# Kernel optimization log

Hardware: AMD Instinct MI355X
Metric: run time of the kernel (lower is better)

## Reference

```python
import jax, jax.numpy as jnp
import numpy as np

EPS = 1e-05

def exp_map_at_origin(v, c):
    sqrt_c = jnp.sqrt(c)
    v_norm = jnp.maximum(jnp.linalg.norm(v, axis=-1, keepdims=True), EPS)
    return (1.0 / sqrt_c) * jnp.tanh(sqrt_c * v_norm) * (v / v_norm)

def log_map_at_origin(y, c):
    sqrt_c = jnp.sqrt(c)
    y_norm = jnp.maximum(jnp.linalg.norm(y, axis=-1, keepdims=True), EPS)
    y_norm_clamped = jnp.minimum(y_norm, 1.0 / sqrt_c - EPS)
    return (1.0 / sqrt_c) * jnp.arctanh(sqrt_c * y_norm_clamped) * (y / y_norm)

def poincare_distance(x, y, c):
    # x, y: [B, H, S, d]; returns [B, H, S, S]
    sqrt_c = jnp.sqrt(c)
    xns = jnp.sum(x * x, axis=-1, keepdims=True)          # [B,H,S,1]
    yns = jnp.sum(y * y, axis=-1, keepdims=True)          # [B,H,S,1]
    xy = jnp.einsum('bhsd,bhtd->bhst', x, y)
    xnsb = xns                                            # broadcast over t
    ynsb = jnp.swapaxes(yns, -2, -1)                      # [B,H,1,S]
    diff_norm_sq = xnsb - 2.0 * xy + ynsb
    denom = jnp.maximum((1.0 - c * xnsb) * (1.0 - c * ynsb), EPS)
    arg = jnp.maximum(1.0 + 2.0 * c * diff_norm_sq / denom, 1.0 + EPS)
    return (1.0 / sqrt_c) * jnp.arccosh(arg)

def setup_inputs() -> dict:
    key = jax.random.key(0)
    ks = jax.random.split(key, 5)
    B, S, D = 2, 1024, 1024
    x = jax.random.normal(ks[0], (B, S, D), dtype=jnp.float32)
    scale = 0.02
    W_q = scale * jax.random.normal(ks[1], (D, D), dtype=jnp.float32)
    W_k = scale * jax.random.normal(ks[2], (D, D), dtype=jnp.float32)
    W_v = scale * jax.random.normal(ks[3], (D, D), dtype=jnp.float32)
    W_o = scale * jax.random.normal(ks[4], (D, D), dtype=jnp.float32)
    return {
        'x': x, 'W_q': W_q, 'W_k': W_k, 'W_v': W_v, 'W_o': W_o,
        'log_c': jnp.zeros((), jnp.float32),
        'beta': jnp.zeros((), jnp.float32),
        'attention_bias': jnp.zeros((), jnp.float32),
    }

def reference(x, W_q, W_k, W_v, W_o, log_c, beta, attention_bias):
    B, S, D = x.shape
    H = 16
    dh = D // H
    c = jax.nn.softplus(log_c)
    beta_pos = jax.nn.softplus(beta)

    def split_heads(t):  # [B,S,D] -> [B,H,S,dh]
        return jnp.transpose(t.reshape(B, S, H, dh), (0, 2, 1, 3))

    q_t = split_heads(x @ W_q.T)
    k_t = split_heads(x @ W_k.T)
    v_t = split_heads(x @ W_v.T)

    q_h = exp_map_at_origin(q_t, c)
    k_h = exp_map_at_origin(k_t, c)
    v_h = exp_map_at_origin(v_t, c)

    dist = poincare_distance(q_h, k_h, c)                 # [B,H,S,S]
    scores = -beta_pos * dist - attention_bias
    weights = jax.nn.softmax(scores, axis=-1)

    v_tan = log_map_at_origin(v_h, c)
    out_tan = jnp.einsum('bhst,bhtd->bhsd', weights, v_tan)
    out_hyp = exp_map_at_origin(out_tan, c)
    out_heads_tan = log_map_at_origin(out_hyp, c)

    concat = jnp.transpose(out_heads_tan, (0, 2, 1, 3)).reshape(B, S, D)
    return concat @ W_o.T
```

## Files before the change

### kernel.cpp

```cpp
#include <hip/hip_runtime.h>
#include <math.h>


#define EPS_ 1e-5f

constexpr int Ss = 1024, Dd = 1024, Hh = 16, DHh = 64;

typedef __attribute__((ext_vector_type(8))) short bf16x8;
typedef __attribute__((ext_vector_type(4))) short s16x4;
typedef __attribute__((ext_vector_type(4))) float f32x4;

__device__ __forceinline__ float softplusf_(float x) {
    return (x > 20.f) ? x : log1pf(expf(x));
}
__device__ __forceinline__ float waveSum64(float v) {
#pragma unroll
    for (int m = 32; m >= 1; m >>= 1) v += __shfl_xor(v, m, 64);
    return v;
}
__device__ __forceinline__ short f2bf(float f) {
    union { float f; unsigned u; } v; v.f = f;
    unsigned r = v.u + 0x7FFFu + ((v.u >> 16) & 1u);
    return (short)(r >> 16);
}
__device__ __forceinline__ float bf2f(unsigned short h) {
    union { unsigned u; float f; } v; v.u = ((unsigned)h) << 16;
    return v.f;
}
__device__ __forceinline__ unsigned pks(short a, short b) {
    return (unsigned)(unsigned short)a | ((unsigned)(unsigned short)b << 16);
}

#if __has_builtin(__builtin_amdgcn_cvt_pk_bf16_f32)
typedef __attribute__((ext_vector_type(2))) __bf16 bfp2;
__device__ __forceinline__ unsigned cvtpk(float a, float b) {
    union { bfp2 v; unsigned u; } x;
    x.v = __builtin_amdgcn_cvt_pk_bf16_f32(a, b);
    return x.u;
}
#else
__device__ __forceinline__ unsigned cvtpk(float a, float b) { return pks(f2bf(a), f2bf(b)); }
#endif

#if __has_builtin(__builtin_amdgcn_sqrtf)
#define FSQRT __builtin_amdgcn_sqrtf
#else
#define FSQRT sqrtf
#endif
#if __has_builtin(__builtin_amdgcn_logf)
#define FLOG2 __builtin_amdgcn_logf
#else
#define FLOG2 __log2f
#endif
#if __has_builtin(__builtin_amdgcn_exp2f)
#define FEXP2 __builtin_amdgcn_exp2f
#else
#define FEXP2 exp2f
#endif

__device__ __forceinline__ void gload_lds16(const short* gp, short* lp) {
    __builtin_amdgcn_global_load_lds(
        (__attribute__((address_space(1))) void*)(void*)(const_cast<short*>(gp)),
        (__attribute__((address_space(3))) void*)(void*)(lp), 16, 0, 0);
}

__global__ __launch_bounds__(256) void split_all(
    const float* __restrict__ x,  const float* __restrict__ Wq,
    const float* __restrict__ Wk, const float* __restrict__ Wv,
    const float* __restrict__ Wo,
    short* __restrict__ xh,  short* __restrict__ wqh,
    short* __restrict__ wkh, short* __restrict__ wvh, short* __restrict__ woh)
{
    int g = blockIdx.x * 256 + threadIdx.x;
    const float* src; short* dst; int base;
    if (g < 524288)       { src = x;  dst = xh;  base = g; }
    else if (g < 786432)  { src = Wq; dst = wqh; base = g - 524288; }
    else if (g < 1048576) { src = Wk; dst = wkh; base = g - 786432; }
    else if (g < 1310720) { src = Wv; dst = wvh; base = g - 1048576; }
    else                  { src = Wo; dst = woh; base = g - 1310720; }
    float4 v = *(const float4*)(src + (size_t)base * 4);
    uint2 hp; hp.x = cvtpk(v.x, v.y); hp.y = cvtpk(v.z, v.w);
    *(uint2*)(dst + (size_t)base * 4) = hp;
}

__global__ __launch_bounds__(256, 3) void gemm_qkv(
    const short* __restrict__ Ap,
    const short* __restrict__ Wq, const short* __restrict__ Wk, const short* __restrict__ Wv,
    short* __restrict__ qh, short* __restrict__ kh, short* __restrict__ vtT,
    float* __restrict__ qnsT, float2* __restrict__ knpk,
    const float* __restrict__ p_logc)
{
    const int z = blockIdx.z;
    const short* Bp = (z == 0) ? Wq : (z == 1 ? Wk : Wv);
    const int K = 1024;

    __shared__ short As[128 * 64];
    __shared__ short Bs[64 * 64];

    const int tid = threadIdx.x;
    const int wv = tid >> 6, lane = tid & 63, quad = lane >> 4, l15 = lane & 15;
    const int bm = blockIdx.y * 128, bn = blockIdx.x * 64;

    const int lr8 = lane >> 3, lc8 = lane & 7;
    const int swz8 = (lc8 ^ lr8) * 8;

    const short* gAl = Ap + (size_t)(bm + lr8) * K + swz8;
    const short* gBl = Bp + (size_t)(bn + lr8) * K + swz8;

    f32x4 acc[2][4];
#pragma unroll
    for (int mt = 0; mt < 2; mt++)
#pragma unroll
        for (int j = 0; j < 4; j++) acc[mt][j] = (f32x4){0.f, 0.f, 0.f, 0.f};

    for (int k0 = 0; k0 < K; k0 += 64) {
        __syncthreads();
#pragma unroll
        for (int i = 0; i < 4; i++)
            gload_lds16(gAl + (size_t)((wv * 4 + i) * 8) * K + k0, &As[(wv * 4 + i) * 512]);
#pragma unroll
        for (int j = 0; j < 2; j++)
            gload_lds16(gBl + (size_t)((wv * 2 + j) * 8) * K + k0, &Bs[(wv * 2 + j) * 512]);
        __syncthreads();
#pragma unroll
        for (int w = 0; w < 2; w++) {
            const int xs = ((w * 4 + quad) ^ (l15 & 7)) * 8;
            bf16x8 fa0 = *(const bf16x8*)&As[(wv * 32 + l15) * 64 + xs];
            bf16x8 fa1 = *(const bf16x8*)&As[(wv * 32 + 16 + l15) * 64 + xs];
#pragma unroll
            for (int nt = 0; nt < 4; nt++) {
                bf16x8 fb = *(const bf16x8*)&Bs[(nt * 16 + l15) * 64 + xs];
                acc[0][nt] = __builtin_amdgcn_mfma_f32_16x16x32_bf16(fa0, fb, acc[0][nt], 0, 0, 0);
                acc[1][nt] = __builtin_amdgcn_mfma_f32_16x16x32_bf16(fa1, fb, acc[1][nt], 0, 0, 0);
            }
        }
    }

    const float c = softplusf_(p_logc[0]);
    const float sc = sqrtf(c);
    const float twoC = 2.f * c;
    const int h0 = blockIdx.x;

    if (z < 2) {
        short* yout = (z == 0) ? qh : kh;
#pragma unroll
        for (int mt = 0; mt < 2; mt++) {
            const int mbase = bm + wv * 32 + mt * 16;
            float fr[4];
#pragma unroll
            for (int r = 0; r < 4; r++) {
                float s2 = 0.f;
#pragma unroll
                for (int nt = 0; nt < 4; nt++) s2 += acc[mt][nt][r] * acc[mt][nt][r];
#pragma unroll
                for (int mk = 1; mk < 16; mk <<= 1) s2 += __shfl_xor(s2, mk, 64);
                float n = fmaxf(sqrtf(s2), EPS_);
                float fac = tanhf(sc * n) / (sc * n);
                fr[r] = fac;
                if (l15 == 0) {
                    int m = mbase + quad * 4 + r;
                    int bI = m >> 10, s = m & 1023;
                    float yns = s2 * fac * fac;
                    if (z == 0) {
                        qnsT[(size_t)(bI * Hh + h0) * Ss + s] = yns;
                    } else {
                        knpk[(size_t)(bI * Hh + h0) * Ss + s]
                            = make_float2(yns, twoC / (1.f - c * yns));
                    }
                }
            }
#pragma unroll
            for (int nt = 0; nt < 4; nt++)
#pragma unroll
                for (int r = 0; r < 4; r++) {
                    int m = mbase + quad * 4 + r;
                    yout[(size_t)m * Dd + bn + nt * 16 + l15] = f2bf(acc[mt][nt][r] * fr[r]);
                }
        }
    } else {
#pragma unroll
        for (int mt = 0; mt < 2; mt++) {
            const int mbase = bm + wv * 32 + mt * 16;
            float tr[4];
#pragma unroll
            for (int r = 0; r < 4; r++) {
                float s2 = 0.f;
#pragma unroll
                for (int nt = 0; nt < 4; nt++) s2 += acc[mt][nt][r] * acc[mt][nt][r];
#pragma unroll
                for (int mk = 1; mk < 16; mk <<= 1) s2 += __shfl_xor(s2, mk, 64);
                float n = fmaxf(sqrtf(s2), EPS_);
                float fac = tanhf(sc * n) / (sc * n);
                float yn = n * fac;
                float ycl = fminf(yn, 1.f / sc - EPS_);
                float f2 = atanhf(sc * ycl) / (sc * fmaxf(yn, EPS_));
                tr[r] = fac * f2;
            }
            const int m0 = mbase + quad * 4;
            const int bI = m0 >> 10, s0 = m0 & 1023;
            const int w6 = s0 & 63;
            const int s0p = (s0 & ~63)
                          | ((w6 >> 5) * 32 + ((w6 & 15) >> 2) * 8 + ((w6 >> 4) & 1) * 4);
#pragma unroll
            for (int nt = 0; nt < 4; nt++) {
                int d = nt * 16 + l15;
                uint2 pk;
                pk.x = cvtpk(acc[mt][nt][0] * tr[0], acc[mt][nt][1] * tr[1]);
                pk.y = cvtpk(acc[mt][nt][2] * tr[2], acc[mt][nt][3] * tr[3]);
                *(uint2*)&vtT[((size_t)(bI * Hh + h0) * DHh + d) * Ss + s0p] = pk;
            }
        }
    }
}

__global__ __launch_bounds__(256) void attn_mfma(
    const short* __restrict__ qh, const short* __restrict__ kh, const short* __restrict__ vtT,
    const float* __restrict__ qnsT, const float2* __restrict__ knpk,
    unsigned short* __restrict__ Opart, float* __restrict__ lpart,
    const float* __restrict__ p_logc, const float* __restrict__ p_beta)
{
    const float c = softplusf_(p_logc[0]);
    const float sc = sqrtf(c);
    const float bp = softplusf_(p_beta[0]);
    const float nkc = -bp / sc;
    const float cap = 2.f * c * 1e5f;
    const float onePlus = 1.f + EPS_;

    const int h = blockIdx.y, b = blockIdx.z;
    const int kr = blockIdx.x & 1, qt = blockIdx.x >> 1;
    const int tid = threadIdx.x;
    const int wv = tid >> 6, lane = tid & 63;
    const int quad = lane >> 4, l15 = lane & 15;
    const int bh = b * Hh + h;
    const int q = qt * 64 + wv * 16 + l15;

    __shared__ short Ks[2][64 * 64];
    __shared__ short Vt[2][64 * 64];

    const short* qb = qh + (size_t)(b * Ss + q) * Dd + h * DHh + quad * 8;
    bf16x8 qf0 = *(const bf16x8*)qb;
    bf16x8 qf1 = *(const bf16x8*)(qb + 32);

    const float qn = qnsT[(size_t)bh * Ss + q];
    const float irq = 1.f / (1.f - c * qn);

    f32x4 O4[4];
#pragma unroll
    for (int nt = 0; nt < 4; nt++) O4[nt] = (f32x4){0.f, 0.f, 0.f, 0.f};
    float lac = 0.f;

    const int tbase = kr * 512;
    const int lr8 = lane >> 3, lc8 = lane & 7;
    const float2* nb = knpk + (size_t)bh * Ss;
    const short* ksb = kh + (size_t)b * Ss * Dd + h * DHh + (lc8 ^ lr8) * 8;
    const short* vsb = vtT + (size_t)bh * DHh * Ss + tbase + (lc8 ^ lr8) * 8;

#pragma unroll
    for (int j = 0; j < 2; j++) {
        const int R = wv * 16 + j * 8;
        gload_lds16(ksb + (size_t)(tbase + R + lr8) * Dd, &Ks[0][R * 64]);
        gload_lds16(vsb + (size_t)(R + lr8) * Ss, &Vt[0][R * 64]);
    }
    __syncthreads();

    const int xsl = (quad ^ (l15 & 7)) * 8;

    for (int ch = 0; ch < 8; ch++) {
        const int cur = ch & 1, nxt = cur ^ 1;
        const int t0 = tbase + ch * 64;

        if (ch < 7) {
#pragma unroll
            for (int j = 0; j < 2; j++) {
                const int R = wv * 16 + j * 8;
                gload_lds16(ksb + (size_t)(tbase + (ch + 1) * 64 + R + lr8) * Dd,
                            &Ks[nxt][R * 64]);
                gload_lds16(vsb + (size_t)(R + lr8) * Ss + (ch + 1) * 64,
                            &Vt[nxt][R * 64]);
            }
        }

        f32x4 n0[4], n1[4];
#pragma unroll
        for (int nt = 0; nt < 4; nt++) {
            const float2* np = nb + t0 + nt * 16 + quad * 4;
            n0[nt] = *(const f32x4*)np;
            n1[nt] = *(const f32x4*)(np + 2);
        }

        f32x4 acc[4];
#pragma unroll
        for (int nt = 0; nt < 4; nt++) {
            bf16x8 k0 = *(const bf16x8*)&Ks[cur][(nt * 16 + l15) * 64 + xsl];
            bf16x8 k1 = *(const bf16x8*)&Ks[cur][(nt * 16 + l15) * 64 + (xsl ^ 32)];
            f32x4 a = (f32x4){0.f, 0.f, 0.f, 0.f};
            a = __builtin_amdgcn_mfma_f32_16x16x32_bf16(k0, qf0, a, 0, 0, 0);
            a = __builtin_amdgcn_mfma_f32_16x16x32_bf16(k1, qf1, a, 0, 0, 0);
            acc[nt] = a;
        }

        bf16x8 v0[4], v1[4];
#pragma unroll
        for (int nt = 0; nt < 4; nt++) {
            v0[nt] = *(const bf16x8*)&Vt[cur][(nt * 16 + l15) * 64 + xsl];
            v1[nt] = *(const bf16x8*)&Vt[cur][(nt * 16 + l15) * 64 + (xsl ^ 32)];
        }

        float sv[4][4];
#pragma unroll
        for (int nt = 0; nt < 4; nt++) {
#pragma unroll
            for (int r = 0; r < 4; r++) {
                float kn   = (r < 2) ? n0[nt][(r & 1) * 2]     : n1[nt][(r & 1) * 2];
                float ik2c = (r < 2) ? n0[nt][(r & 1) * 2 + 1] : n1[nt][(r & 1) * 2 + 1];
                float dns = (qn + kn) - 2.f * acc[nt][r];
                float co  = fminf(irq * ik2c, cap);
                float arg = fmaxf(fmaf(co, dns, 1.f), onePlus);
                float u   = arg + FSQRT(fmaf(arg, arg, -1.f));
                float p   = FEXP2(nkc * FLOG2(u));
                sv[nt][r] = p;
                lac += p;
            }
        }

        union { unsigned u[4]; bf16x8 v; } p0, p1;
        p0.u[0] = cvtpk(sv[0][0], sv[0][1]); p0.u[1] = cvtpk(sv[0][2], sv[0][3]);
        p0.u[2] = cvtpk(sv[1][0], sv[1][1]); p0.u[3] = cvtpk(sv[1][2], sv[1][3]);
        p1.u[0] = cvtpk(sv[2][0], sv[2][1]); p1.u[1] = cvtpk(sv[2][2], sv[2][3]);
        p1.u[2] = cvtpk(sv[3][0], sv[3][1]); p1.u[3] = cvtpk(sv[3][2], sv[3][3]);

#pragma unroll
        for (int nt = 0; nt < 4; nt++) {
            O4[nt] = __builtin_amdgcn_mfma_f32_16x16x32_bf16(v0[nt], p0.v, O4[nt], 0, 0, 0);
            O4[nt] = __builtin_amdgcn_mfma_f32_16x16x32_bf16(v1[nt], p1.v, O4[nt], 0, 0, 0);
        }

        if (ch < 7) __syncthreads();
    }

    lac += __shfl_xor(lac, 16, 64);
    lac += __shfl_xor(lac, 32, 64);
    unsigned short* ob = Opart + (((size_t)bh * 2 + kr) * Ss + q) * DHh;
#pragma unroll
    for (int nt = 0; nt < 4; nt++) {
        uint2 pk;
        pk.x = cvtpk(O4[nt][0], O4[nt][1]);
        pk.y = cvtpk(O4[nt][2], O4[nt][3]);
        *(uint2*)(ob + nt * 16 + quad * 4) = pk;
    }
    if (lane < 16)
        lpart[((size_t)bh * 2 + kr) * Ss + qt * 64 + wv * 16 + lane] = lac;
}

__global__ __launch_bounds__(256) void attn_combine(
    const unsigned short* __restrict__ Opart, const float* __restrict__ lpart,
    short* __restrict__ ccb, const float* __restrict__ p_logc)
{
    const float c = softplusf_(p_logc[0]);
    const float sc = sqrtf(c);
    const int wv = threadIdx.x >> 6, d = threadIdx.x & 63;
    const int task = blockIdx.x * 4 + wv;
    const int bh = task >> 10, s = task & 1023;

    float O = 0.f, l = 0.f;
#pragma unroll
    for (int k = 0; k < 2; k++) {
        O += bf2f(Opart[(((size_t)bh * 2 + k) * Ss + s) * DHh + d]);
        l += lpart[((size_t)bh * 2 + k) * Ss + s];
    }
    float ot = O / l;

    float t2 = waveSum64(ot * ot);
    float n = fmaxf(sqrtf(t2), EPS_);
    float fac = tanhf(sc * n) / (sc * n);
    float y2 = t2 * fac * fac;
    float yn = fmaxf(sqrtf(y2), EPS_);
    float ycl = fminf(yn, 1.f / sc - EPS_);
    float fac2 = atanhf(sc * ycl) / (sc * yn);
    float tot = fac * fac2;

    int b = bh >> 4, hh = bh & 15;
    ccb[(size_t)(b * Ss + s) * Dd + hh * DHh + d] = f2bf(ot * tot);
}

__global__ __launch_bounds__(256, 6) void gemm_out(
    const short* __restrict__ Ap, const short* __restrict__ Bp,
    float* __restrict__ Cp)
{
    const int K = 1024, N = 1024;
    __shared__ short As[64 * 64];
    __shared__ short Bs[64 * 64];
    const int tid = threadIdx.x;
    const int wv = tid >> 6, lane = tid & 63, quad = lane >> 4, l15 = lane & 15;
    const int bm = blockIdx.y * 64, bn = blockIdx.x * 64;

    const int lr8 = lane >> 3, lc8 = lane & 7;
    const int swz8 = (lc8 ^ lr8) * 8;

    const short* gAl = Ap + (size_t)(bm + lr8) * K + swz8;
    const short* gBl = Bp + (size_t)(bn + lr8) * K + swz8;

    f32x4 acc[4];
#pragma unroll
    for (int j = 0; j < 4; j++) acc[j] = (f32x4){0.f, 0.f, 0.f, 0.f};

    for (int k0 = 0; k0 < K; k0 += 64) {
        __syncthreads();
#pragma unroll
        for (int j = 0; j < 2; j++) {
            gload_lds16(gAl + (size_t)((wv * 2 + j) * 8) * K + k0, &As[(wv * 2 + j) * 512]);
            gload_lds16(gBl + (size_t)((wv * 2 + j) * 8) * K + k0, &Bs[(wv * 2 + j) * 512]);
        }
        __syncthreads();
#pragma unroll
        for (int w = 0; w < 2; w++) {
            const int xs = ((w * 4 + quad) ^ (l15 & 7)) * 8;
            bf16x8 fa = *(const bf16x8*)&As[(wv * 16 + l15) * 64 + xs];
#pragma unroll
            for (int nt = 0; nt < 4; nt++) {
                bf16x8 fb = *(const bf16x8*)&Bs[(nt * 16 + l15) * 64 + xs];
                acc[nt] = __builtin_amdgcn_mfma_f32_16x16x32_bf16(fa, fb, acc[nt], 0, 0, 0);
            }
        }
    }
#pragma unroll
    for (int nt = 0; nt < 4; nt++)
#pragma unroll
        for (int r = 0; r < 4; r++)
            Cp[(size_t)(bm + wv * 16 + quad * 4 + r) * N + bn + nt * 16 + l15] = acc[nt][r];
}

extern "C" void kernel_launch(void* const* d_in, const int* in_sizes, int n_in,
                              void* d_out, int out_size, void* d_ws, size_t ws_size,
                              hipStream_t stream)
{
    const float* x    = (const float*)d_in[0];
    const float* Wq   = (const float*)d_in[1];
    const float* Wk   = (const float*)d_in[2];
    const float* Wv   = (const float*)d_in[3];
    const float* Wo   = (const float*)d_in[4];
    const float* logc = (const float*)d_in[5];
    const float* beta = (const float*)d_in[6];
    float* out = (float*)d_out;

    const size_t M2 = 2097152, M1 = 1048576;
    short* ws    = (short*)d_ws;
    short* xh    = ws;
    short* wqh   = xh + M2;
    short* wkh   = wqh + M1;
    short* wvh   = wkh + M1;
    short* woh   = wvh + M1;
    short* qh    = woh + M1;
    short* kh    = qh + M2;
    short* vtT   = kh + M2;
    float* qnsT  = (float*)(vtT + M2);
    float2* knpk = (float2*)(qnsT + 32768);
    float* lpart = (float*)(knpk + 32768);
    unsigned short* Opart = (unsigned short*)(lpart + 65536);
    short* ccb   = xh;

    split_all<<<dim3(6144), 256, 0, stream>>>(x, Wq, Wk, Wv, Wo, xh, wqh, wkh, wvh, woh);
    gemm_qkv<<<dim3(16, 16, 3), 256, 0, stream>>>(xh, wqh, wkh, wvh,
        qh, kh, vtT, qnsT, knpk, logc);
    attn_mfma<<<dim3(32, 16, 2), 256, 0, stream>>>(qh, kh, vtT, qnsT, knpk,
        Opart, lpart, logc, beta);
    attn_combine<<<dim3(8192), 256, 0, stream>>>(Opart, lpart, ccb, logc);
    gemm_out<<<dim3(16, 32), 256, 0, stream>>>(ccb, woh, out);
}
```

Before: 174.1 us.

## Fuse split-K attention combine into attention kernel via intra-block LDS reduction

The two key-range halves that were separate blocks now run as two wave groups inside one 512-thread block. The partial outputs and row sums are reduced through shared memory, and the exp/log map epilogue is applied in-kernel, so the attn_combine launch and the Opart/lpart global round trip go away. s_setprio is also raised around the MFMA sections to favor matrix issue. The cost is a larger block with twice the LDS, half the number of blocks, and an extra shared-memory reduction step at the end.

```diff
diff --git a/kernel.cpp b/kernel.cpp
--- a/kernel.cpp
+++ b/kernel.cpp
@@ -12,20 +12,11 @@
 
 __device__ __forceinline__ float softplusf_(float x) {
     return (x > 20.f) ? x : log1pf(expf(x));
-}
-__device__ __forceinline__ float waveSum64(float v) {
-#pragma unroll
-    for (int m = 32; m >= 1; m >>= 1) v += __shfl_xor(v, m, 64);
-    return v;
 }
 __device__ __forceinline__ short f2bf(float f) {
     union { float f; unsigned u; } v; v.f = f;
     unsigned r = v.u + 0x7FFFu + ((v.u >> 16) & 1u);
     return (short)(r >> 16);
-}
-__device__ __forceinline__ float bf2f(unsigned short h) {
-    union { unsigned u; float f; } v; v.u = ((unsigned)h) << 16;
-    return v.f;
 }
 __device__ __forceinline__ unsigned pks(short a, short b) {
     return (unsigned)(unsigned short)a | ((unsigned)(unsigned short)b << 16);
@@ -213,10 +204,10 @@
     }
 }
 
-__global__ __launch_bounds__(256) void attn_mfma(
+__global__ __launch_bounds__(512) void attn_mfma(
     const short* __restrict__ qh, const short* __restrict__ kh, const short* __restrict__ vtT,
     const float* __restrict__ qnsT, const float2* __restrict__ knpk,
-    unsigned short* __restrict__ Opart, float* __restrict__ lpart,
+    short* __restrict__ ccb,
     const float* __restrict__ p_logc, const float* __restrict__ p_beta)
 {
     const float c = softplusf_(p_logc[0]);
@@ -226,16 +217,16 @@
     const float cap = 2.f * c * 1e5f;
     const float onePlus = 1.f + EPS_;
 
-    const int h = blockIdx.y, b = blockIdx.z;
-    const int kr = blockIdx.x & 1, qt = blockIdx.x >> 1;
+    const int h = blockIdx.y, b = blockIdx.z, qt = blockIdx.x;
     const int tid = threadIdx.x;
     const int wv = tid >> 6, lane = tid & 63;
+    const int g = wv >> 2, w4 = wv & 3;
     const int quad = lane >> 4, l15 = lane & 15;
     const int bh = b * Hh + h;
-    const int q = qt * 64 + wv * 16 + l15;
-
-    __shared__ short Ks[2][64 * 64];
-    __shared__ short Vt[2][64 * 64];
+    const int q = qt * 64 + w4 * 16 + l15;
+
+    __shared__ short Ks[2][2][4096];
+    __shared__ short Vt[2][2][4096];
 
     const short* qb = qh + (size_t)(b * Ss + q) * Dd + h * DHh + quad * 8;
     bf16x8 qf0 = *(const bf16x8*)qb;
@@ -249,7 +240,7 @@
     for (int nt = 0; nt < 4; nt++) O4[nt] = (f32x4){0.f, 0.f, 0.f, 0.f};
     float lac = 0.f;
 
-    const int tbase = kr * 512;
+    const int tbase = g * 512;
     const int lr8 = lane >> 3, lc8 = lane & 7;
     const float2* nb = knpk + (size_t)bh * Ss;
     const short* ksb = kh + (size_t)b * Ss * Dd + h * DHh + (lc8 ^ lr8) * 8;
@@ -257,9 +248,9 @@
 
 #pragma unroll
     for (int j = 0; j < 2; j++) {
-        const int R = wv * 16 + j * 8;
-        gload_lds16(ksb + (size_t)(tbase + R + lr8) * Dd, &Ks[0][R * 64]);
-        gload_lds16(vsb + (size_t)(R + lr8) * Ss, &Vt[0][R * 64]);
+        const int R = w4 * 16 + j * 8;
+        gload_lds16(ksb + (size_t)(tbase + R + lr8) * Dd, &Ks[g][0][R * 64]);
+        gload_lds16(vsb + (size_t)(R + lr8) * Ss, &Vt[g][0][R * 64]);
     }
     __syncthreads();
 
@@ -272,11 +263,11 @@
         if (ch < 7) {
 #pragma unroll
             for (int j = 0; j < 2; j++) {
-                const int R = wv * 16 + j * 8;
+                const int R = w4 * 16 + j * 8;
                 gload_lds16(ksb + (size_t)(tbase + (ch + 1) * 64 + R + lr8) * Dd,
-                            &Ks[nxt][R * 64]);
+                            &Ks[g][nxt][R * 64]);
                 gload_lds16(vsb + (size_t)(R + lr8) * Ss + (ch + 1) * 64,
-                            &Vt[nxt][R * 64]);
+                            &Vt[g][nxt][R * 64]);
             }
         }
 
@@ -289,21 +280,23 @@
         }
 
         f32x4 acc[4];
-#pragma unroll
-        for (int nt = 0; nt < 4; nt++) {
-            bf16x8 k0 = *(const bf16x8*)&Ks[cur][(nt * 16 + l15) * 64 + xsl];
-            bf16x8 k1 = *(const bf16x8*)&Ks[cur][(nt * 16 + l15) * 64 + (xsl ^ 32)];
+        __builtin_amdgcn_s_setprio(1);
+#pragma unroll
+        for (int nt = 0; nt < 4; nt++) {
+            bf16x8 k0 = *(const bf16x8*)&Ks[g][cur][(nt * 16 + l15) * 64 + xsl];
+            bf16x8 k1 = *(const bf16x8*)&Ks[g][cur][(nt * 16 + l15) * 64 + (xsl ^ 32)];
             f32x4 a = (f32x4){0.f, 0.f, 0.f, 0.f};
             a = __builtin_amdgcn_mfma_f32_16x16x32_bf16(k0, qf0, a, 0, 0, 0);
             a = __builtin_amdgcn_mfma_f32_16x16x32_bf16(k1, qf1, a, 0, 0, 0);
             acc[nt] = a;
         }
+        __builtin_amdgcn_s_setprio(0);
 
         bf16x8 v0[4], v1[4];
 #pragma unroll
         for (int nt = 0; nt < 4; nt++) {
-            v0[nt] = *(const bf16x8*)&Vt[cur][(nt * 16 + l15) * 64 + xsl];
-            v1[nt] = *(const bf16x8*)&Vt[cur][(nt * 16 + l15) * 64 + (xsl ^ 32)];
+            v0[nt] = *(const bf16x8*)&Vt[g][cur][(nt * 16 + l15) * 64 + xsl];
+            v1[nt] = *(const bf16x8*)&Vt[g][cur][(nt * 16 + l15) * 64 + (xsl ^ 32)];
         }
 
         float sv[4][4];
@@ -329,58 +322,66 @@
         p1.u[0] = cvtpk(sv[2][0], sv[2][1]); p1.u[1] = cvtpk(sv[2][2], sv[2][3]);
         p1.u[2] = cvtpk(sv[3][0], sv[3][1]); p1.u[3] = cvtpk(sv[3][2], sv[3][3]);
 
+        __builtin_amdgcn_s_setprio(1);
 #pragma unroll
         for (int nt = 0; nt < 4; nt++) {
             O4[nt] = __builtin_amdgcn_mfma_f32_16x16x32_bf16(v0[nt], p0.v, O4[nt], 0, 0, 0);
             O4[nt] = __builtin_amdgcn_mfma_f32_16x16x32_bf16(v1[nt], p1.v, O4[nt], 0, 0, 0);
         }
+        __builtin_amdgcn_s_setprio(0);
 
         if (ch < 7) __syncthreads();
     }
 
     lac += __shfl_xor(lac, 16, 64);
     lac += __shfl_xor(lac, 32, 64);
-    unsigned short* ob = Opart + (((size_t)bh * 2 + kr) * Ss + q) * DHh;
-#pragma unroll
-    for (int nt = 0; nt < 4; nt++) {
-        uint2 pk;
-        pk.x = cvtpk(O4[nt][0], O4[nt][1]);
-        pk.y = cvtpk(O4[nt][2], O4[nt][3]);
-        *(uint2*)(ob + nt * 16 + quad * 4) = pk;
-    }
-    if (lane < 16)
-        lpart[((size_t)bh * 2 + kr) * Ss + qt * 64 + wv * 16 + lane] = lac;
-}
-
-__global__ __launch_bounds__(256) void attn_combine(
-    const unsigned short* __restrict__ Opart, const float* __restrict__ lpart,
-    short* __restrict__ ccb, const float* __restrict__ p_logc)
-{
-    const float c = softplusf_(p_logc[0]);
-    const float sc = sqrtf(c);
-    const int wv = threadIdx.x >> 6, d = threadIdx.x & 63;
-    const int task = blockIdx.x * 4 + wv;
-    const int bh = task >> 10, s = task & 1023;
-
-    float O = 0.f, l = 0.f;
-#pragma unroll
-    for (int k = 0; k < 2; k++) {
-        O += bf2f(Opart[(((size_t)bh * 2 + k) * Ss + s) * DHh + d]);
-        l += lpart[((size_t)bh * 2 + k) * Ss + s];
-    }
-    float ot = O / l;
-
-    float t2 = waveSum64(ot * ot);
-    float n = fmaxf(sqrtf(t2), EPS_);
-    float fac = tanhf(sc * n) / (sc * n);
-    float y2 = t2 * fac * fac;
-    float yn = fmaxf(sqrtf(y2), EPS_);
-    float ycl = fminf(yn, 1.f / sc - EPS_);
-    float fac2 = atanhf(sc * ycl) / (sc * yn);
-    float tot = fac * fac2;
-
-    int b = bh >> 4, hh = bh & 15;
-    ccb[(size_t)(b * Ss + s) * Dd + hh * DHh + d] = f2bf(ot * tot);
+
+    float* Ored = (float*)&Ks[0][0][0];
+    float* lred = (float*)&Vt[0][0][0];
+    __syncthreads();
+    if (g == 1) {
+#pragma unroll
+        for (int nt = 0; nt < 4; nt++)
+#pragma unroll
+            for (int r = 0; r < 4; r++)
+                Ored[((w4 * 4 + nt) * 16 + (quad * 4 + r)) * 16 + l15] = O4[nt][r];
+        if (lane < 16) lred[w4 * 16 + lane] = lac;
+    }
+    __syncthreads();
+
+    if (g == 0) {
+        const float lt = lac + lred[w4 * 16 + l15];
+        const float il = 1.f / lt;
+        float ot[4][4], t2 = 0.f;
+#pragma unroll
+        for (int nt = 0; nt < 4; nt++)
+#pragma unroll
+            for (int r = 0; r < 4; r++) {
+                float v = (O4[nt][r]
+                    + Ored[((w4 * 4 + nt) * 16 + (quad * 4 + r)) * 16 + l15]) * il;
+                ot[nt][r] = v;
+                t2 += v * v;
+            }
+        t2 += __shfl_xor(t2, 16, 64);
+        t2 += __shfl_xor(t2, 32, 64);
+
+        float n = fmaxf(sqrtf(t2), EPS_);
+        float fac = tanhf(sc * n) / (sc * n);
+        float y2 = t2 * fac * fac;
+        float yn = fmaxf(sqrtf(y2), EPS_);
+        float ycl = fminf(yn, 1.f / sc - EPS_);
+        float fac2 = atanhf(sc * ycl) / (sc * yn);
+        float tot = fac * fac2;
+
+        short* ob = ccb + (size_t)(b * Ss + q) * Dd + h * DHh;
+#pragma unroll
+        for (int nt = 0; nt < 4; nt++) {
+            uint2 pk;
+            pk.x = cvtpk(ot[nt][0] * tot, ot[nt][1] * tot);
+            pk.y = cvtpk(ot[nt][2] * tot, ot[nt][3] * tot);
+            *(uint2*)(ob + nt * 16 + quad * 4) = pk;
+        }
+    }
 }
 
 __global__ __launch_bounds__(256, 6) void gemm_out(
@@ -455,15 +456,12 @@
     short* vtT   = kh + M2;
     float* qnsT  = (float*)(vtT + M2);
     float2* knpk = (float2*)(qnsT + 32768);
-    float* lpart = (float*)(knpk + 32768);
-    unsigned short* Opart = (unsigned short*)(lpart + 65536);
     short* ccb   = xh;
 
     split_all<<<dim3(6144), 256, 0, stream>>>(x, Wq, Wk, Wv, Wo, xh, wqh, wkh, wvh, woh);
     gemm_qkv<<<dim3(16, 16, 3), 256, 0, stream>>>(xh, wqh, wkh, wvh,
         qh, kh, vtT, qnsT, knpk, logc);
-    attn_mfma<<<dim3(32, 16, 2), 256, 0, stream>>>(qh, kh, vtT, qnsT, knpk,
-        Opart, lpart, logc, beta);
-    attn_combine<<<dim3(8192), 256, 0, stream>>>(Opart, lpart, ccb, logc);
+    attn_mfma<<<dim3(16, 16, 2), 512, 0, stream>>>(qh, kh, vtT, qnsT, knpk,
+        ccb, logc, beta);
     gemm_out<<<dim3(16, 32), 256, 0, stream>>>(ccb, woh, out);
 }
```

New measurement: 158.3 us. 1.1x faster.
